# Performance work log

Measured on AMD Instinct MI355X. Metric: run time of the kernel, lower is better.

Reference implementation:

```python
import jax, jax.numpy as jnp
import numpy as np

IN_DIM = 256
K = 64
NB = 64  # num_blocks
N = NB * K
BATCH = 4096
DT = 0.05
TAU_EPS = 1e-6


def setup_inputs() -> dict:
    key = jax.random.key(0)
    ks = jax.random.split(key, 10)
    def xavier(k_, shape, fan_in, fan_out):
        lim = np.sqrt(6.0 / (fan_in + fan_out))
        return jax.random.uniform(k_, shape, jnp.float32, -lim, lim)
    return {
        "y": jax.random.normal(ks[0], (BATCH, N), jnp.float32),
        "u_t": jax.random.normal(ks[1], (BATCH, IN_DIM), jnp.float32),
        "tau_raw": jnp.zeros((N,), jnp.float32),
        "W_in_w": xavier(ks[2], (K, IN_DIM), IN_DIM, K),
        "W_in_b": jnp.zeros((K,), jnp.float32),
        "W_fwd_w": xavier(ks[3], (NB - 1, K, K), K, K),
        "W_fwd_b": jnp.zeros((NB - 1, K), jnp.float32),
        "W_rec_w": xavier(ks[4], (NB, K, K), K, K),
        "W_rec_b": jnp.zeros((NB, K), jnp.float32),
        "E_l": xavier(ks[5], (NB, K, K), K, K),
        "E_l_r": xavier(ks[6], (NB, K, K), K, K),
    }


def reference(y, u_t, tau_raw, W_in_w, W_in_b, W_fwd_w, W_fwd_b, W_rec_w, W_rec_b, E_l, E_l_r):
    yb = y.reshape(-1, NB, K)  # [batch, B, k]
    tau = jax.nn.softplus(tau_raw).reshape(NB, K) + TAU_EPS  # [B, k]
    # input drive for block 0 (torch Linear: x @ W^T + b)
    net0 = jnp.tanh(u_t @ W_in_w.T + W_in_b)  # [batch, k]
    # forward coupling for blocks 1..B-1, batched over blocks
    prev = yb[:, :-1, :]  # [batch, B-1, k]
    net_fwd = jnp.tanh(jnp.einsum('bji,joi->bjo', prev, W_fwd_w) + W_fwd_b)
    net_out = jnp.concatenate([net0[:, None, :], net_fwd], axis=1)  # [batch, B, k]
    # recurrent coupling, all blocks
    net_rec = jnp.tanh(jnp.einsum('bji,joi->bjo', yb, W_rec_w) + W_rec_b)
    decay = 1.0 / tau + jnp.abs(net_out) + jnp.abs(net_rec)  # [batch, B, k]
    drive = jnp.einsum('joi,bji->bjo', E_l, net_out) + jnp.einsum('joi,bji->bjo', E_l_r, net_rec)
    y_new = (yb + DT * drive) / (1.0 + DT * decay)
    return y_new.reshape(-1, N)
```

## Files before the change

kernel.cpp:

```cpp
#include <hip/hip_runtime.h>


#define IN_DIM 256
#define K 64
#define NB 64
#define BATCH 4096
#define NTOT (NB * K)
#define DTC 0.05f
#define TAU_EPS 1e-6f
#define LDSTR 72
#define NMATS 259
#define WS_W_OFF 16384

typedef __bf16 bf16;
typedef bf16 bf16x8 __attribute__((ext_vector_type(8)));
typedef float f32x4 __attribute__((ext_vector_type(4)));

__device__ __forceinline__ float fast_tanh(float x) {
    float e = __expf(2.0f * x);
    return 1.0f - 2.0f * __builtin_amdgcn_rcpf(e + 1.0f);
}

__device__ __forceinline__ void load_afrag(const float* __restrict__ rowp,
                                           bf16x8& f0, bf16x8& f1) {
    float4 a0 = *(const float4*)(rowp);
    float4 a1 = *(const float4*)(rowp + 4);
    float4 a2 = *(const float4*)(rowp + 32);
    float4 a3 = *(const float4*)(rowp + 36);
    f0 = (bf16x8){ (bf16)a0.x, (bf16)a0.y, (bf16)a0.z, (bf16)a0.w,
                   (bf16)a1.x, (bf16)a1.y, (bf16)a1.z, (bf16)a1.w };
    f1 = (bf16x8){ (bf16)a2.x, (bf16)a2.y, (bf16)a2.z, (bf16)a2.w,
                   (bf16)a3.x, (bf16)a3.y, (bf16)a3.z, (bf16)a3.w };
}

__global__ __launch_bounds__(256)
void pack_kernel(const float* __restrict__ W_in_w, const float* __restrict__ W_fwd_w,
                 const float* __restrict__ W_rec_w, const float* __restrict__ E_l,
                 const float* __restrict__ E_l_r, const float* __restrict__ tau_raw,
                 void* __restrict__ ws) {
    int gid = blockIdx.x * 256 + threadIdx.x;
    float* invTau = (float*)ws;
    bf16* pw = (bf16*)((char*)ws + WS_W_OFF);
    if (gid < NMATS * 512) {
        int m    = gid >> 9;
        int r    = gid & 511;
        int ct   = r >> 7;
        int kh   = (r >> 6) & 1;
        int lane = r & 63;
        int n  = ct * 16 + (lane & 15);
        int k0 = kh * 32 + (lane >> 4) * 8;
        const float* src;
        if      (m < 64)  src = W_rec_w + (size_t)m * 4096         + n * 64  + k0;
        else if (m < 127) src = W_fwd_w + (size_t)(m - 64) * 4096  + n * 64  + k0;
        else if (m < 191) src = E_l     + (size_t)(m - 127) * 4096 + n * 64  + k0;
        else if (m < 255) src = E_l_r   + (size_t)(m - 191) * 4096 + n * 64  + k0;
        else              src = W_in_w  + (size_t)n * IN_DIM + (m - 255) * 64 + k0;
        float4 a = *(const float4*)src;
        float4 b = *(const float4*)(src + 4);
        bf16x8 o = { (bf16)a.x, (bf16)a.y, (bf16)a.z, (bf16)a.w,
                     (bf16)b.x, (bf16)b.y, (bf16)b.z, (bf16)b.w };
        *(bf16x8*)(pw + (size_t)gid * 8) = o;
    } else if (gid < NMATS * 512 + NTOT) {
        int i = gid - NMATS * 512;
        float x = tau_raw[i];
        float sp = (x > 15.0f) ? x : log1pf(__expf(x));
        invTau[i] = 1.0f / (sp + TAU_EPS);
    }
}

__global__ __launch_bounds__(512, 4)
void ltcn_main(const float* __restrict__ y, const float* __restrict__ u_t,
               const float* __restrict__ W_in_b, const float* __restrict__ W_fwd_b,
               const float* __restrict__ W_rec_b, const void* __restrict__ ws,
               float* __restrict__ out) {
    __shared__ bf16 sNo[128 * LDSTR];
    __shared__ bf16 sNr[128 * LDSTR];

    const float* invTau = (const float*)ws;
    const bf16*  pw     = (const bf16*)((const char*)ws + WS_W_OFF);

    const int tid  = threadIdx.x;
    const int j    = blockIdx.y;
    const int b0   = blockIdx.x * 128;
    const int wave = tid >> 6;
    const int lane = tid & 63;
    const int quad = lane >> 4;
    const int l16  = lane & 15;
    const int am   = wave * 16 + l16;
    const int boff = quad * 8;

    bf16x8 yc0, yc1, yp0, yp1;
    load_afrag(y + (size_t)(b0 + am) * NTOT + j * K + boff, yc0, yc1);
    if (j != 0) load_afrag(y + (size_t)(b0 + am) * NTOT + (j - 1) * K + boff, yp0, yp1);
    else        load_afrag(u_t + (size_t)(b0 + am) * IN_DIM + boff, yp0, yp1);

    float brv[4], bfv[4], itv[4];
#pragma unroll
    for (int ct = 0; ct < 4; ++ct) {
        int n = ct * 16 + l16;
        brv[ct] = W_rec_b[j * K + n];
        itv[ct] = invTau[j * K + n];
        bfv[ct] = (j == 0) ? W_in_b[n] : W_fwd_b[(j - 1) * K + n];
    }

    const bf16* mrec = pw + (size_t)j * 4096;
    f32x4 accR[4] = {};
    {
        bf16x8 B0[4], B1[4];
#pragma unroll
        for (int ct = 0; ct < 4; ++ct) {
            B0[ct] = *(const bf16x8*)(mrec + ((ct * 2 + 0) * 64 + lane) * 8);
            B1[ct] = *(const bf16x8*)(mrec + ((ct * 2 + 1) * 64 + lane) * 8);
        }
#pragma unroll
        for (int ct = 0; ct < 4; ++ct) {
            accR[ct] = __builtin_amdgcn_mfma_f32_16x16x32_bf16(yc0, B0[ct], accR[ct], 0, 0, 0);
            accR[ct] = __builtin_amdgcn_mfma_f32_16x16x32_bf16(yc1, B1[ct], accR[ct], 0, 0, 0);
        }
    }

    f32x4 accF[4] = {};
    if (j != 0) {
        const bf16* mfwd = pw + (size_t)(64 + j - 1) * 4096;
        bf16x8 B0[4], B1[4];
#pragma unroll
        for (int ct = 0; ct < 4; ++ct) {
            B0[ct] = *(const bf16x8*)(mfwd + ((ct * 2 + 0) * 64 + lane) * 8);
            B1[ct] = *(const bf16x8*)(mfwd + ((ct * 2 + 1) * 64 + lane) * 8);
        }
#pragma unroll
        for (int ct = 0; ct < 4; ++ct) {
            accF[ct] = __builtin_amdgcn_mfma_f32_16x16x32_bf16(yp0, B0[ct], accF[ct], 0, 0, 0);
            accF[ct] = __builtin_amdgcn_mfma_f32_16x16x32_bf16(yp1, B1[ct], accF[ct], 0, 0, 0);
        }
    } else {
#pragma unroll 1
        for (int kc = 0; kc < 4; ++kc) {
            if (kc) load_afrag(u_t + (size_t)(b0 + am) * IN_DIM + kc * 64 + boff, yp0, yp1);
            const bf16* mwin = pw + (size_t)(255 + kc) * 4096;
            bf16x8 B0[4], B1[4];
#pragma unroll
            for (int ct = 0; ct < 4; ++ct) {
                B0[ct] = *(const bf16x8*)(mwin + ((ct * 2 + 0) * 64 + lane) * 8);
                B1[ct] = *(const bf16x8*)(mwin + ((ct * 2 + 1) * 64 + lane) * 8);
            }
#pragma unroll
            for (int ct = 0; ct < 4; ++ct) {
                accF[ct] = __builtin_amdgcn_mfma_f32_16x16x32_bf16(yp0, B0[ct], accF[ct], 0, 0, 0);
                accF[ct] = __builtin_amdgcn_mfma_f32_16x16x32_bf16(yp1, B1[ct], accF[ct], 0, 0, 0);
            }
        }
    }

    const bf16* mel  = pw + (size_t)(127 + j) * 4096;
    const bf16* melr = pw + (size_t)(191 + j) * 4096;
    bf16x8 Bo0[4], Bo1[4];
#pragma unroll
    for (int ct = 0; ct < 4; ++ct) {
        Bo0[ct] = *(const bf16x8*)(mel + ((ct * 2 + 0) * 64 + lane) * 8);
        Bo1[ct] = *(const bf16x8*)(mel + ((ct * 2 + 1) * 64 + lane) * 8);
    }

    float absum[4][4];
#pragma unroll
    for (int ct = 0; ct < 4; ++ct) {
#pragma unroll
        for (int r = 0; r < 4; ++r) {
            float no = fast_tanh(accF[ct][r] + bfv[ct]);
            float nr = fast_tanh(accR[ct][r] + brv[ct]);
            accF[ct][r] = no;
            accR[ct][r] = nr;
            absum[ct][r] = itv[ct] + fabsf(no) + fabsf(nr);
        }
    }

    bf16* bandO = sNo + wave * 16 * LDSTR;
    bf16* bandR = sNr + wave * 16 * LDSTR;
#pragma unroll
    for (int ct = 0; ct < 4; ++ct) {
#pragma unroll
        for (int r = 0; r < 4; ++r) {
            int mrow = quad * 4 + r;
            int n = ct * 16 + l16;
            bandO[mrow * LDSTR + n] = (bf16)accF[ct][r];
            bandR[mrow * LDSTR + n] = (bf16)accR[ct][r];
        }
    }

    const bf16* apO = bandO + l16 * LDSTR + boff;
    const bf16* apR = bandR + l16 * LDSTR + boff;
    bf16x8 aO0 = *(const bf16x8*)apO, aO1 = *(const bf16x8*)(apO + 32);
    bf16x8 aR0 = *(const bf16x8*)apR, aR1 = *(const bf16x8*)(apR + 32);

    bf16x8 Be0[4], Be1[4];
#pragma unroll
    for (int ct = 0; ct < 4; ++ct) {
        Be0[ct] = *(const bf16x8*)(melr + ((ct * 2 + 0) * 64 + lane) * 8);
        Be1[ct] = *(const bf16x8*)(melr + ((ct * 2 + 1) * 64 + lane) * 8);
    }

    f32x4 accD[4] = {};
#pragma unroll
    for (int ct = 0; ct < 4; ++ct) {
        accD[ct] = __builtin_amdgcn_mfma_f32_16x16x32_bf16(aO0, Bo0[ct], accD[ct], 0, 0, 0);
        accD[ct] = __builtin_amdgcn_mfma_f32_16x16x32_bf16(aO1, Bo1[ct], accD[ct], 0, 0, 0);
    }

    float ye[4][4];
    const float* yep = y + (size_t)(b0 + wave * 16 + quad * 4) * NTOT + (size_t)j * K + l16;
#pragma unroll
    for (int ct = 0; ct < 4; ++ct)
#pragma unroll
        for (int r = 0; r < 4; ++r)
            ye[ct][r] = yep[(size_t)r * NTOT + ct * 16];

#pragma unroll
    for (int ct = 0; ct < 4; ++ct) {
        accD[ct] = __builtin_amdgcn_mfma_f32_16x16x32_bf16(aR0, Be0[ct], accD[ct], 0, 0, 0);
        accD[ct] = __builtin_amdgcn_mfma_f32_16x16x32_bf16(aR1, Be1[ct], accD[ct], 0, 0, 0);
    }

#pragma unroll
    for (int ct = 0; ct < 4; ++ct) {
#pragma unroll
        for (int r = 0; r < 4; ++r) {
            size_t gi = (size_t)(b0 + wave * 16 + quad * 4 + r) * NTOT + j * K + ct * 16 + l16;
            out[gi] = (ye[ct][r] + DTC * accD[ct][r])
                      * __builtin_amdgcn_rcpf(1.0f + DTC * absum[ct][r]);
        }
    }
}

extern "C" void kernel_launch(void* const* d_in, const int* in_sizes, int n_in,
                              void* d_out, int out_size, void* d_ws, size_t ws_size,
                              hipStream_t stream) {
    const float* y       = (const float*)d_in[0];
    const float* u_t     = (const float*)d_in[1];
    const float* tau_raw = (const float*)d_in[2];
    const float* W_in_w  = (const float*)d_in[3];
    const float* W_in_b  = (const float*)d_in[4];
    const float* W_fwd_w = (const float*)d_in[5];
    const float* W_fwd_b = (const float*)d_in[6];
    const float* W_rec_w = (const float*)d_in[7];
    const float* W_rec_b = (const float*)d_in[8];
    const float* E_l     = (const float*)d_in[9];
    const float* E_l_r   = (const float*)d_in[10];
    float* out = (float*)d_out;

    int pack_threads = NMATS * 512 + NTOT;
    hipLaunchKernelGGL(pack_kernel, dim3((pack_threads + 255) / 256), dim3(256),
                       0, stream,
                       W_in_w, W_fwd_w, W_rec_w, E_l, E_l_r, tau_raw, d_ws);

    dim3 grid(BATCH / 128, NB);
    hipLaunchKernelGGL(ltcn_main, grid, dim3(512), 0, stream,
                       y, u_t, W_in_b, W_fwd_b, W_rec_b, d_ws, out);
}
```

Measured before the change: 171.9 us.

## Stage block weight matrices in LDS and reuse a swizzled net buffer

Each workgroup now loads the four 64x64 bf16 weight matrices (rec, fwd or first W_in chunk, E_l, E_l_r) cooperatively into shared memory once, with one sync. All eight waves then read B fragments from LDS, where before each wave fetched the same matrices from global memory on its own. The padded two-buffer net staging is replaced by one XOR-swizzled 64-wide band per wave that is reused for net_out and then net_rec. This cuts LDS footprint and avoids bank conflicts, but adds a barrier and increases LDS usage to 48KB, which may reduce occupancy.

```diff
diff --git a/kernel.cpp b/kernel.cpp
--- a/kernel.cpp
+++ b/kernel.cpp
@@ -8,7 +8,6 @@
 #define NTOT (NB * K)
 #define DTC 0.05f
 #define TAU_EPS 1e-6f
-#define LDSTR 72
 #define NMATS 259
 #define WS_W_OFF 16384
 
@@ -73,8 +72,8 @@
                const float* __restrict__ W_in_b, const float* __restrict__ W_fwd_b,
                const float* __restrict__ W_rec_b, const void* __restrict__ ws,
                float* __restrict__ out) {
-    __shared__ bf16 sNo[128 * LDSTR];
-    __shared__ bf16 sNr[128 * LDSTR];
+    __shared__ bf16 sW[4 * 4096];
+    __shared__ bf16 sNet[8 * 1024];
 
     const float* invTau = (const float*)ws;
     const bf16*  pw     = (const bf16*)((const char*)ws + WS_W_OFF);
@@ -103,62 +102,40 @@
         bfv[ct] = (j == 0) ? W_in_b[n] : W_fwd_b[(j - 1) * K + n];
     }
 
-    const bf16* mrec = pw + (size_t)j * 4096;
-    f32x4 accR[4] = {};
     {
-        bf16x8 B0[4], B1[4];
-#pragma unroll
-        for (int ct = 0; ct < 4; ++ct) {
-            B0[ct] = *(const bf16x8*)(mrec + ((ct * 2 + 0) * 64 + lane) * 8);
-            B1[ct] = *(const bf16x8*)(mrec + ((ct * 2 + 1) * 64 + lane) * 8);
-        }
-#pragma unroll
-        for (int ct = 0; ct < 4; ++ct) {
-            accR[ct] = __builtin_amdgcn_mfma_f32_16x16x32_bf16(yc0, B0[ct], accR[ct], 0, 0, 0);
-            accR[ct] = __builtin_amdgcn_mfma_f32_16x16x32_bf16(yc1, B1[ct], accR[ct], 0, 0, 0);
-        }
-    }
-
-    f32x4 accF[4] = {};
-    if (j != 0) {
-        const bf16* mfwd = pw + (size_t)(64 + j - 1) * 4096;
-        bf16x8 B0[4], B1[4];
-#pragma unroll
-        for (int ct = 0; ct < 4; ++ct) {
-            B0[ct] = *(const bf16x8*)(mfwd + ((ct * 2 + 0) * 64 + lane) * 8);
-            B1[ct] = *(const bf16x8*)(mfwd + ((ct * 2 + 1) * 64 + lane) * 8);
-        }
-#pragma unroll
-        for (int ct = 0; ct < 4; ++ct) {
-            accF[ct] = __builtin_amdgcn_mfma_f32_16x16x32_bf16(yp0, B0[ct], accF[ct], 0, 0, 0);
-            accF[ct] = __builtin_amdgcn_mfma_f32_16x16x32_bf16(yp1, B1[ct], accF[ct], 0, 0, 0);
-        }
-    } else {
+        int m1 = (j != 0) ? (64 + j - 1) : 255;
+        *(bf16x8*)(sW +    0     + tid * 8) = *(const bf16x8*)(pw + (size_t)j          * 4096 + tid * 8);
+        *(bf16x8*)(sW + 1 * 4096 + tid * 8) = *(const bf16x8*)(pw + (size_t)m1         * 4096 + tid * 8);
+        *(bf16x8*)(sW + 2 * 4096 + tid * 8) = *(const bf16x8*)(pw + (size_t)(127 + j)  * 4096 + tid * 8);
+        *(bf16x8*)(sW + 3 * 4096 + tid * 8) = *(const bf16x8*)(pw + (size_t)(191 + j)  * 4096 + tid * 8);
+    }
+    __syncthreads();
+
+    f32x4 accR[4] = {}, accF[4] = {};
+#pragma unroll
+    for (int ct = 0; ct < 4; ++ct) {
+        bf16x8 br0 = *(const bf16x8*)(sW +            ((ct * 2 + 0) * 64 + lane) * 8);
+        bf16x8 br1 = *(const bf16x8*)(sW +            ((ct * 2 + 1) * 64 + lane) * 8);
+        accR[ct] = __builtin_amdgcn_mfma_f32_16x16x32_bf16(yc0, br0, accR[ct], 0, 0, 0);
+        accR[ct] = __builtin_amdgcn_mfma_f32_16x16x32_bf16(yc1, br1, accR[ct], 0, 0, 0);
+        bf16x8 bf0 = *(const bf16x8*)(sW + 1 * 4096 + ((ct * 2 + 0) * 64 + lane) * 8);
+        bf16x8 bf1 = *(const bf16x8*)(sW + 1 * 4096 + ((ct * 2 + 1) * 64 + lane) * 8);
+        accF[ct] = __builtin_amdgcn_mfma_f32_16x16x32_bf16(yp0, bf0, accF[ct], 0, 0, 0);
+        accF[ct] = __builtin_amdgcn_mfma_f32_16x16x32_bf16(yp1, bf1, accF[ct], 0, 0, 0);
+    }
+    if (j == 0) {
 #pragma unroll 1
-        for (int kc = 0; kc < 4; ++kc) {
-            if (kc) load_afrag(u_t + (size_t)(b0 + am) * IN_DIM + kc * 64 + boff, yp0, yp1);
+        for (int kc = 1; kc < 4; ++kc) {
+            load_afrag(u_t + (size_t)(b0 + am) * IN_DIM + kc * 64 + boff, yp0, yp1);
             const bf16* mwin = pw + (size_t)(255 + kc) * 4096;
-            bf16x8 B0[4], B1[4];
 #pragma unroll
             for (int ct = 0; ct < 4; ++ct) {
-                B0[ct] = *(const bf16x8*)(mwin + ((ct * 2 + 0) * 64 + lane) * 8);
-                B1[ct] = *(const bf16x8*)(mwin + ((ct * 2 + 1) * 64 + lane) * 8);
+                bf16x8 b0 = *(const bf16x8*)(mwin + ((ct * 2 + 0) * 64 + lane) * 8);
+                bf16x8 b1 = *(const bf16x8*)(mwin + ((ct * 2 + 1) * 64 + lane) * 8);
+                accF[ct] = __builtin_amdgcn_mfma_f32_16x16x32_bf16(yp0, b0, accF[ct], 0, 0, 0);
+                accF[ct] = __builtin_amdgcn_mfma_f32_16x16x32_bf16(yp1, b1, accF[ct], 0, 0, 0);
             }
-#pragma unroll
-            for (int ct = 0; ct < 4; ++ct) {
-                accF[ct] = __builtin_amdgcn_mfma_f32_16x16x32_bf16(yp0, B0[ct], accF[ct], 0, 0, 0);
-                accF[ct] = __builtin_amdgcn_mfma_f32_16x16x32_bf16(yp1, B1[ct], accF[ct], 0, 0, 0);
-            }
-        }
-    }
-
-    const bf16* mel  = pw + (size_t)(127 + j) * 4096;
-    const bf16* melr = pw + (size_t)(191 + j) * 4096;
-    bf16x8 Bo0[4], Bo1[4];
-#pragma unroll
-    for (int ct = 0; ct < 4; ++ct) {
-        Bo0[ct] = *(const bf16x8*)(mel + ((ct * 2 + 0) * 64 + lane) * 8);
-        Bo1[ct] = *(const bf16x8*)(mel + ((ct * 2 + 1) * 64 + lane) * 8);
+        }
     }
 
     float absum[4][4];
@@ -174,37 +151,37 @@
         }
     }
 
-    bf16* bandO = sNo + wave * 16 * LDSTR;
-    bf16* bandR = sNr + wave * 16 * LDSTR;
-#pragma unroll
-    for (int ct = 0; ct < 4; ++ct) {
-#pragma unroll
-        for (int r = 0; r < 4; ++r) {
-            int mrow = quad * 4 + r;
-            int n = ct * 16 + l16;
-            bandO[mrow * LDSTR + n] = (bf16)accF[ct][r];
-            bandR[mrow * LDSTR + n] = (bf16)accR[ct][r];
-        }
-    }
-
-    const bf16* apO = bandO + l16 * LDSTR + boff;
-    const bf16* apR = bandR + l16 * LDSTR + boff;
-    bf16x8 aO0 = *(const bf16x8*)apO, aO1 = *(const bf16x8*)(apO + 32);
-    bf16x8 aR0 = *(const bf16x8*)apR, aR1 = *(const bf16x8*)(apR + 32);
-
-    bf16x8 Be0[4], Be1[4];
-#pragma unroll
-    for (int ct = 0; ct < 4; ++ct) {
-        Be0[ct] = *(const bf16x8*)(melr + ((ct * 2 + 0) * 64 + lane) * 8);
-        Be1[ct] = *(const bf16x8*)(melr + ((ct * 2 + 1) * 64 + lane) * 8);
-    }
+    bf16* band = sNet + wave * 1024;
+    const int sw = (l16 & 7) << 3;
+    const bf16* a0p = band + l16 * 64 + ((boff     ) ^ sw);
+    const bf16* a1p = band + l16 * 64 + ((32 + boff) ^ sw);
+
+#pragma unroll
+    for (int ct = 0; ct < 4; ++ct)
+#pragma unroll
+        for (int r = 0; r < 4; ++r) {
+            int rr = quad * 4 + r;
+            band[rr * 64 + ((ct * 16 + l16) ^ ((rr & 7) << 3))] = (bf16)accF[ct][r];
+        }
+    bf16x8 aO0 = *(const bf16x8*)a0p, aO1 = *(const bf16x8*)a1p;
 
     f32x4 accD[4] = {};
 #pragma unroll
     for (int ct = 0; ct < 4; ++ct) {
-        accD[ct] = __builtin_amdgcn_mfma_f32_16x16x32_bf16(aO0, Bo0[ct], accD[ct], 0, 0, 0);
-        accD[ct] = __builtin_amdgcn_mfma_f32_16x16x32_bf16(aO1, Bo1[ct], accD[ct], 0, 0, 0);
-    }
+        bf16x8 b0 = *(const bf16x8*)(sW + 2 * 4096 + ((ct * 2 + 0) * 64 + lane) * 8);
+        bf16x8 b1 = *(const bf16x8*)(sW + 2 * 4096 + ((ct * 2 + 1) * 64 + lane) * 8);
+        accD[ct] = __builtin_amdgcn_mfma_f32_16x16x32_bf16(aO0, b0, accD[ct], 0, 0, 0);
+        accD[ct] = __builtin_amdgcn_mfma_f32_16x16x32_bf16(aO1, b1, accD[ct], 0, 0, 0);
+    }
+
+#pragma unroll
+    for (int ct = 0; ct < 4; ++ct)
+#pragma unroll
+        for (int r = 0; r < 4; ++r) {
+            int rr = quad * 4 + r;
+            band[rr * 64 + ((ct * 16 + l16) ^ ((rr & 7) << 3))] = (bf16)accR[ct][r];
+        }
+    bf16x8 aR0 = *(const bf16x8*)a0p, aR1 = *(const bf16x8*)a1p;
 
     float ye[4][4];
     const float* yep = y + (size_t)(b0 + wave * 16 + quad * 4) * NTOT + (size_t)j * K + l16;
@@ -216,8 +193,10 @@
 
 #pragma unroll
     for (int ct = 0; ct < 4; ++ct) {
-        accD[ct] = __builtin_amdgcn_mfma_f32_16x16x32_bf16(aR0, Be0[ct], accD[ct], 0, 0, 0);
-        accD[ct] = __builtin_amdgcn_mfma_f32_16x16x32_bf16(aR1, Be1[ct], accD[ct], 0, 0, 0);
+        bf16x8 b0 = *(const bf16x8*)(sW + 3 * 4096 + ((ct * 2 + 0) * 64 + lane) * 8);
+        bf16x8 b1 = *(const bf16x8*)(sW + 3 * 4096 + ((ct * 2 + 1) * 64 + lane) * 8);
+        accD[ct] = __builtin_amdgcn_mfma_f32_16x16x32_bf16(aR0, b0, accD[ct], 0, 0, 0);
+        accD[ct] = __builtin_amdgcn_mfma_f32_16x16x32_bf16(aR1, b1, accD[ct], 0, 0, 0);
     }
 
 #pragma unroll
```

New measurement: 162.2 us. -5.6%, faster.
